# Kernel optimization log

Hardware: AMD Instinct MI355X
Metric: run time of the kernel (lower is better)

Reference implementation:

```python
import jax, jax.numpy as jnp
import numpy as np

EPS = 1e-8


def setup_inputs() -> dict:
    key = jax.random.key(0)
    ks = jax.random.split(key, 8)
    B, N, D = 8, 2048, 768
    H, R = 768, 4
    return {
        "x": jax.random.normal(ks[0], (B, N, D), dtype=jnp.float32),
        "scale": jnp.ones((D,), dtype=jnp.float32),
        "U": jax.random.normal(ks[1], (H, R), dtype=jnp.float32) * 0.02,
        "V": jax.random.normal(ks[2], (H, R), dtype=jnp.float32) * 0.02,
        "S_param": jax.random.normal(ks[3], (H, H), dtype=jnp.float32) * 0.01,
        "Bm": jax.random.normal(ks[4], (H, D), dtype=jnp.float32) * (1.0 / np.sqrt(D)),
        "Cm": jax.random.normal(ks[5], (D, H), dtype=jnp.float32) * (1.0 / np.sqrt(H)),
        "gate_w": jax.random.normal(ks[6], (D, D), dtype=jnp.float32) * (1.0 / np.sqrt(D)),
        "gate_b": jnp.zeros((D,), dtype=jnp.float32),
        "alpha": jnp.full((1,), 0.1, dtype=jnp.float32),
    }


def reference(x, scale, U, V, S_param, Bm, Cm, gate_w, gate_b, alpha):
    B, N, D = x.shape
    H = Bm.shape[0]
    # A = diag(A_diag) + U V^T + (S - S^T); A_diag is a fixed buffer.
    A_diag = -jnp.linspace(1.0, float(H), H, dtype=x.dtype) / H
    A = jnp.diag(A_diag) + U @ V.T + (S_param - S_param.T)
    At = A.T  # apply as h @ A.T
    # RMSNorm
    rms = jnp.sqrt(jnp.mean(x * x, axis=-1, keepdims=True) + EPS)
    xn = x / rms * scale
    # Precompute input injections u_t = x_t @ B.T for all t: (N, B, H)
    u = jnp.einsum('bnd,hd->nbh', xn, Bm)

    def step(h, ut):
        h = h @ At + ut
        return h, h @ Cm.T  # (B, D)

    h0 = jnp.zeros((B, H), dtype=x.dtype)
    _, y_fwd = jax.lax.scan(step, h0, u)                 # (N, B, D)
    _, y_bwd = jax.lax.scan(step, h0, u, reverse=True)   # (N, B, D), indexed in time order
    y = 0.5 * (y_fwd + y_bwd)
    y = jnp.swapaxes(y, 0, 1)  # (B, N, D)
    # Gate
    g = jax.nn.sigmoid(jnp.einsum('bnd,ed->bne', xn, gate_w) + gate_b)
    y = y * g
    # Skip (dropout is identity in eval)
    return x + alpha * y
```

## Files before the change

kernel.cpp:

```cpp
#include <hip/hip_runtime.h>


typedef short  bfrag __attribute__((ext_vector_type(8)));
typedef float  ffrag __attribute__((ext_vector_type(4)));
typedef float  f4    __attribute__((ext_vector_type(4)));
typedef short  s4v   __attribute__((ext_vector_type(4)));

#define DEV static __device__ __forceinline__
#define Hn 768
#define FLS 132

DEV unsigned short f2bf(float f) {
  unsigned u = __float_as_uint(f);
  u += 0x7fffu + ((u >> 16) & 1u);
  return (unsigned short)(u >> 16);
}
DEV float bf2f(unsigned short s) { return __uint_as_float(((unsigned)s) << 16); }

DEV ffrag mfma16(bfrag a, bfrag b, ffrag c) {
  return __builtin_amdgcn_mfma_f32_16x16x32_bf16(a, b, c, 0, 0, 0);
}

DEV void glds16(const unsigned short* g, unsigned short* l) {
  __builtin_amdgcn_global_load_lds(
      (const __attribute__((address_space(1))) unsigned int*)g,
      (__attribute__((address_space(3))) unsigned int*)l, 16, 0, 0);
}

template<int N> DEV void vwait() {
  if constexpr (N == 0)      asm volatile("s_waitcnt vmcnt(0)" ::: "memory");
  else if constexpr (N == 4) asm volatile("s_waitcnt vmcnt(4)" ::: "memory");
  else if constexpr (N == 8) asm volatile("s_waitcnt vmcnt(8)" ::: "memory");
}

union BF8 { bfrag v; unsigned short u[8]; };

__global__ __launch_bounds__(256) void k_abuild(
    const float* __restrict__ U, const float* __restrict__ V,
    const float* __restrict__ S, const float* __restrict__ Bm,
    const float* __restrict__ Cm, const float* __restrict__ gw,
    float* __restrict__ Af, float* __restrict__ AfT,
    unsigned short* __restrict__ Abf,
    unsigned short* __restrict__ Bmb, unsigned short* __restrict__ Cmb,
    unsigned short* __restrict__ gwb, unsigned short* __restrict__ zp) {
  int i = blockIdx.x;
  int task = blockIdx.y;
  if (task == 0) {
    float u0 = U[i*4+0], u1 = U[i*4+1], u2 = U[i*4+2], u3 = U[i*4+3];
    for (int j = threadIdx.x; j < Hn; j += 256) {
      float a = u0*V[j*4+0] + u1*V[j*4+1] + u2*V[j*4+2] + u3*V[j*4+3]
              + S[i*Hn+j] - S[j*Hn+i];
      if (i == j) a += -(float)(i+1) / 768.0f;
      Af[i*Hn+j]  = a;
      AfT[j*Hn+i] = a;
      Abf[i*Hn+j] = f2bf(a);
    }
    if (i == 0) for (int j = threadIdx.x; j < 1024; j += 256) zp[j] = 0;
  } else {
    const float* src = (task==1) ? Bm : (task==2) ? Cm : gw;
    unsigned short* dst = (task==1) ? Bmb : (task==2) ? Cmb : gwb;
    for (int j = threadIdx.x; j < Hn; j += 256) dst[i*Hn+j] = f2bf(src[i*Hn+j]);
  }
}

__global__ __launch_bounds__(256) void k_rms(
    const float* __restrict__ x, const float* __restrict__ scale,
    unsigned short* __restrict__ xn) {
  int row  = blockIdx.x * 4 + (threadIdx.x >> 6);
  int lane = threadIdx.x & 63;
  int b = row >> 11, t = row & 2047;
  const float* xr = x + (long)row * Hn;
  float v[12];
  float ss = 0.f;
#pragma unroll
  for (int j = 0; j < 12; ++j) { v[j] = xr[lane + j*64]; ss += v[j]*v[j]; }
#pragma unroll
  for (int off = 1; off < 64; off <<= 1) ss += __shfl_xor(ss, off);
  float inv = 1.0f / sqrtf(ss / 768.0f + 1e-8f);
  unsigned short* dst = xn + ((long)t * 8 + b) * Hn;
#pragma unroll
  for (int j = 0; j < 12; ++j) dst[lane + j*64] = f2bf(v[j] * inv * scale[lane + j*64]);
}

__global__ __launch_bounds__(512) void k_sq(
    const float* __restrict__ X, const float* __restrict__ XT,
    float* __restrict__ Z, float* __restrict__ ZT,
    unsigned short* __restrict__ Zbf) {
  int tid = threadIdx.x, lane = tid & 63, w = tid >> 6;
  int mw = w >> 2, nw = w & 3, l15 = lane & 15, lhi = lane >> 4;
  int rb = blockIdx.x * 64, cb = blockIdx.y * 128;
  ffrag acc[2][2] = {};
  for (int kt = 0; kt < 24; ++kt) {
    int k0 = kt*32 + lhi*8;
    BF8 ah[2], al[2], bh[2], bl[2];
#pragma unroll
    for (int mt = 0; mt < 2; ++mt) {
      const f4* p = (const f4*)(X + (long)(rb + mw*32 + mt*16 + l15) * Hn + k0);
      f4 x0 = p[0], x1 = p[1];
#pragma unroll
      for (int j = 0; j < 8; ++j) {
        float f = (j < 4) ? x0[j] : x1[j-4];
        unsigned short h = f2bf(f);
        ah[mt].u[j] = h; al[mt].u[j] = f2bf(f - bf2f(h));
      }
    }
#pragma unroll
    for (int nt = 0; nt < 2; ++nt) {
      const f4* p = (const f4*)(XT + (long)(cb + nw*32 + nt*16 + l15) * Hn + k0);
      f4 x0 = p[0], x1 = p[1];
#pragma unroll
      for (int j = 0; j < 8; ++j) {
        float f = (j < 4) ? x0[j] : x1[j-4];
        unsigned short h = f2bf(f);
        bh[nt].u[j] = h; bl[nt].u[j] = f2bf(f - bf2f(h));
      }
    }
#pragma unroll
    for (int mt = 0; mt < 2; ++mt)
#pragma unroll
      for (int nt = 0; nt < 2; ++nt) {
        acc[mt][nt] = mfma16(ah[mt].v, bh[nt].v, acc[mt][nt]);
        acc[mt][nt] = mfma16(ah[mt].v, bl[nt].v, acc[mt][nt]);
        acc[mt][nt] = mfma16(al[mt].v, bh[nt].v, acc[mt][nt]);
      }
  }
#pragma unroll
  for (int mt = 0; mt < 2; ++mt)
#pragma unroll
    for (int nt = 0; nt < 2; ++nt)
#pragma unroll
      for (int q = 0; q < 4; ++q) {
        int grow = rb + mw*32 + mt*16 + lhi*4 + q;
        int gcol = cb + nw*32 + nt*16 + l15;
        float vv = acc[mt][nt][q];
        Z[(long)grow*Hn + gcol] = vv;
        ZT[(long)gcol*Hn + grow] = vv;
        Zbf[(long)grow*Hn + gcol] = f2bf(vv);
      }
}

template<int MODE>
__global__ __launch_bounds__(256) void k_gemm(
    const unsigned short* __restrict__ A0s, const unsigned short* __restrict__ A1s,
    const unsigned short* __restrict__ B0s, const unsigned short* __restrict__ B1s,
    const unsigned short* __restrict__ res, unsigned short* __restrict__ outb,
    const unsigned short* __restrict__ zp, int sh, int dup,
    const float* __restrict__ gb, const float* __restrict__ alpha,
    const float* __restrict__ x, float* __restrict__ outf) {
  constexpr int NA   = (MODE == 0) ? 1 : 2;
  constexpr int NB   = (MODE == 2) ? 2 : 1;
  constexpr int NT   = NA + NB;
  constexpr int NBUF = (MODE == 0) ? 3 : 2;
  constexpr int NL   = 2 * NT;

  __shared__ __align__(16) char smem[NBUF * NT * 8192];
  unsigned short* ldsb = (unsigned short*)smem;

  const int tid = threadIdx.x, lane = tid & 63, w = tid >> 6;
  const int l15 = lane & 15, lhi = lane >> 4;
  const int wr = w >> 1, wc = w & 1;

  const int nwg = gridDim.x;
  const int q8 = nwg >> 3, r8 = nwg & 7, xcd = blockIdx.x & 7, fo = blockIdx.x >> 3;
  const int wg = (xcd < r8 ? xcd*(q8+1) : r8*(q8+1) + (xcd - r8)*q8) + fo;
  const int cb = wg % 6, rbk = wg / 6;
  const long r0 = (long)rbk * 128;
  const long bc0 = (long)cb * 128;
  const int dir = (MODE == 0 && r0 >= 16384) ? 1 : 0;

  bool skip = false;
  if (MODE == 0 && sh > 0)
    skip = dir ? (r0 >= 32768 - sh) : (r0 + 128 <= sh);

  const int rowin = lane >> 2, ch = lane & 3;
  long gA[NA][2]; bool vA[NA][2]; long gB[NB][2]; int lbase[2];
#pragma unroll
  for (int jj = 0; jj < 2; ++jj) {
    const int inst = w*2 + jj;
    const int r = inst*16 + rowin;
    const int c = ch ^ ((r ^ (r >> 2)) & 3);
    lbase[jj] = inst * 512;
#pragma unroll
    for (int s = 0; s < NA; ++s) {
      long gr; bool ok = true;
      if (MODE == 0) {
        gr = r0 + r + (dir ? sh : -sh);
        ok = dir ? (gr < 32768) : (gr >= 0);
      } else if (MODE == 1) {
        if (s == 0) { gr = r0 + r - sh; ok = (gr >= 0); }
        else        { gr = r0 + r + 16384 + sh; ok = (gr < 32768); }
      } else {
        gr = r0 + r;
      }
      vA[s][jj] = ok; gA[s][jj] = gr * Hn + c*8;
    }
#pragma unroll
    for (int s = 0; s < NB; ++s)
      gB[s][jj] = (bc0 + r) * Hn + c*8;
  }

  auto stage = [&](int buf, int kt) {
    const int ko = kt * 32;
    unsigned short* dst = ldsb + buf * (NT * 4096);
#pragma unroll
    for (int jj = 0; jj < 2; ++jj) {
#pragma unroll
      for (int s = 0; s < NA; ++s) {
        const unsigned short* src0 = (MODE == 2 && s == 1) ? A1s : A0s;
        const unsigned short* g = vA[s][jj] ? (src0 + gA[s][jj] + ko) : zp;
        glds16(g, dst + s*4096 + lbase[jj]);
      }
#pragma unroll
      for (int s = 0; s < NB; ++s) {
        const unsigned short* src0 = (s == 0) ? B0s : B1s;
        glds16(src0 + gB[s][jj] + ko, dst + (NA + s)*4096 + lbase[jj]);
      }
    }
  };

  ffrag acc[4][4] = {};
  ffrag accZ[(MODE == 2) ? 4 : 1][(MODE == 2) ? 4 : 1] = {};
  const int cx = (lhi ^ ((l15 ^ (l15 >> 2)) & 3)) * 8;

  if (!skip) {
    if (MODE == 0) {
      stage(0, 0); stage(1, 1);
      int cur = 0;
      for (int kt = 0; kt < 24; ++kt) {
        if (kt < 23) vwait<4>(); else vwait<0>();
        __builtin_amdgcn_s_barrier();
        if (kt + 2 <= 23) stage((kt + 2) % 3, kt + 2);
        const unsigned short* L = ldsb + cur * (NT * 4096);
        bfrag a0[4], b0[4];
#pragma unroll
        for (int mt = 0; mt < 4; ++mt)
          a0[mt] = *(const bfrag*)&L[(wr*64 + mt*16 + l15)*32 + cx];
#pragma unroll
        for (int nt = 0; nt < 4; ++nt)
          b0[nt] = *(const bfrag*)&L[4096 + (wc*64 + nt*16 + l15)*32 + cx];
#pragma unroll
        for (int mt = 0; mt < 4; ++mt)
#pragma unroll
          for (int nt = 0; nt < 4; ++nt)
            acc[mt][nt] = mfma16(a0[mt], b0[nt], acc[mt][nt]);
        cur = (cur == 2) ? 0 : cur + 1;
      }
    } else {
      stage(0, 0);
      int cur = 0;
      for (int kt = 0; kt < 24; ++kt) {
        vwait<0>();
        __builtin_amdgcn_s_barrier();
        if (kt < 23) stage(cur ^ 1, kt + 1);
        const unsigned short* L = ldsb + cur * (NT * 4096);
        bfrag a[2][4], b0[4], b1[4];
#pragma unroll
        for (int mt = 0; mt < 4; ++mt) {
          const int row = wr*64 + mt*16 + l15;
          a[0][mt] = *(const bfrag*)&L[row*32 + cx];
          a[1][mt] = *(const bfrag*)&L[4096 + row*32 + cx];
        }
#pragma unroll
        for (int nt = 0; nt < 4; ++nt) {
          const int row = wc*64 + nt*16 + l15;
          b0[nt] = *(const bfrag*)&L[2*4096 + row*32 + cx];
          if (MODE == 2) b1[nt] = *(const bfrag*)&L[3*4096 + row*32 + cx];
        }
#pragma unroll
        for (int mt = 0; mt < 4; ++mt)
#pragma unroll
          for (int nt = 0; nt < 4; ++nt) {
            if (MODE == 1) {
              acc[mt][nt] = mfma16(a[0][mt], b0[nt], acc[mt][nt]);
              acc[mt][nt] = mfma16(a[1][mt], b0[nt], acc[mt][nt]);
            } else {
              acc[mt][nt]  = mfma16(a[0][mt], b0[nt], acc[mt][nt]);
              accZ[mt][nt] = mfma16(a[1][mt], b1[nt], accZ[mt][nt]);
            }
          }
        cur ^= 1;
      }
    }
  }

  if (MODE == 2) {
    const float al = alpha[0];
    float gvals[4];
#pragma unroll
    for (int nt = 0; nt < 4; ++nt) gvals[nt] = gb[bc0 + wc*64 + nt*16 + l15];
#pragma unroll
    for (int mt = 0; mt < 4; ++mt)
#pragma unroll
      for (int nt = 0; nt < 4; ++nt)
#pragma unroll
        for (int q = 0; q < 4; ++q) {
          float z = accZ[mt][nt][q] + gvals[nt];
          float g = 1.0f / (1.0f + __expf(-z));
          acc[mt][nt][q] *= al * 0.5f * g;
        }
  }

  float* fl = (float*)smem;
#pragma unroll
  for (int hh = 0; hh < 2; ++hh) {
    __syncthreads();
    if (wr == hh) {
#pragma unroll
      for (int mt = 0; mt < 4; ++mt)
#pragma unroll
        for (int nt = 0; nt < 4; ++nt)
#pragma unroll
          for (int q = 0; q < 4; ++q)
            fl[(mt*16 + lhi*4 + q)*FLS + wc*64 + nt*16 + l15] = acc[mt][nt][q];
    }
    __syncthreads();
    for (int i = tid; i < 2048; i += 256) {
      const int row = i >> 5;
      const int cc  = (i & 31) << 2;
      f4 v = *(const f4*)&fl[row*FLS + cc];
      const long grow = r0 + hh*64 + row;
      const long gcol = bc0 + cc;
      const long go = grow * Hn + gcol;
      if (MODE == 0) {
        if (res) {
          s4v rv = *(const s4v*)&res[go];
#pragma unroll
          for (int j = 0; j < 4; ++j) v[j] += bf2f(((unsigned short*)&rv)[j]);
        }
        s4v ov;
#pragma unroll
        for (int j = 0; j < 4; ++j) ((unsigned short*)&ov)[j] = f2bf(v[j]);
        *(s4v*)&outb[go] = ov;
        if (dup) *(s4v*)&outb[go + (long)16384*Hn] = ov;
      } else if (MODE == 1) {
        s4v ra = *(const s4v*)&res[go];
        s4v rb2 = *(const s4v*)&res[go + (long)16384*Hn];
#pragma unroll
        for (int j = 0; j < 4; ++j)
          v[j] += bf2f(((unsigned short*)&ra)[j]) + bf2f(((unsigned short*)&rb2)[j]);
        s4v ov;
#pragma unroll
        for (int j = 0; j < 4; ++j) ((unsigned short*)&ov)[j] = f2bf(v[j]);
        *(s4v*)&outb[go] = ov;
      } else {
        const long t = grow >> 3, b = grow & 7;
        const long o = (b*2048 + t)*Hn + gcol;
        f4 xv = *(const f4*)&x[o];
        f4 ov;
#pragma unroll
        for (int j = 0; j < 4; ++j) ov[j] = xv[j] + v[j];
        *(f4*)&outf[o] = ov;
      }
    }
  }
}

extern "C" void kernel_launch(void* const* d_in, const int* in_sizes, int n_in,
                              void* d_out, int out_size, void* d_ws, size_t ws_size,
                              hipStream_t stream) {
  const float* x     = (const float*)d_in[0];
  const float* scale = (const float*)d_in[1];
  const float* U     = (const float*)d_in[2];
  const float* V     = (const float*)d_in[3];
  const float* S     = (const float*)d_in[4];
  const float* Bm    = (const float*)d_in[5];
  const float* Cm    = (const float*)d_in[6];
  const float* gw    = (const float*)d_in[7];
  const float* gb    = (const float*)d_in[8];
  const float* alpha = (const float*)d_in[9];
  float* out = (float*)d_out;

  char* p = (char*)d_ws;
  auto alloc = [&](size_t sz) { char* r = p; p += (sz + 255) & ~(size_t)255; return r; };

  const size_t SZ_X  = (size_t)32768 * Hn * sizeof(unsigned short);
  const size_t SZ_BF = (size_t)16384 * Hn * sizeof(unsigned short);
  const size_t SZ_M  = (size_t)Hn * Hn * sizeof(float);
  const size_t SZ_MB = (size_t)Hn * Hn * sizeof(unsigned short);

  unsigned short* xn = (unsigned short*)alloc(SZ_BF);
  unsigned short* XA = (unsigned short*)alloc(SZ_X);
  unsigned short* XB = (unsigned short*)alloc(SZ_X);
  float* Af  = (float*)alloc(SZ_M);
  float* AfT = (float*)alloc(SZ_M);
  float* P1  = (float*)alloc(SZ_M);
  float* P1T = (float*)alloc(SZ_M);
  float* P2  = (float*)alloc(SZ_M);
  float* P2T = (float*)alloc(SZ_M);
  unsigned short* Abf = (unsigned short*)alloc(SZ_MB);
  unsigned short* Ab[10];
  for (int i = 0; i < 10; ++i) Ab[i] = (unsigned short*)alloc(SZ_MB);
  unsigned short* Bmb = (unsigned short*)alloc(SZ_MB);
  unsigned short* Cmb = (unsigned short*)alloc(SZ_MB);
  unsigned short* gwb = (unsigned short*)alloc(SZ_MB);
  unsigned short* zp  = (unsigned short*)alloc(1024 * sizeof(unsigned short));

  if ((size_t)(p - (char*)d_ws) > ws_size) return;

  k_abuild<<<dim3(768, 4), 256, 0, stream>>>(U, V, S, Bm, Cm, gw,
      Af, AfT, Abf, Bmb, Cmb, gwb, zp);
  k_rms<<<4096, 256, 0, stream>>>(x, scale, xn);

  const float* sx = Af; const float* sxt = AfT;
  float* za = P1; float* zat = P1T; float* zb = P2; float* zbt = P2T;
  for (int i = 0; i < 10; ++i) {
    k_sq<<<dim3(12, 6), 512, 0, stream>>>(sx, sxt, za, zat, Ab[i]);
    sx = za; sxt = zat;
    float* t1 = za; float* t2 = zat; za = zb; zat = zbt; zb = t1; zbt = t2;
  }

  k_gemm<0><<<768, 256, 0, stream>>>(xn, nullptr, Bmb, nullptr, nullptr, XA,
      zp, 0, 1, nullptr, nullptr, nullptr, nullptr);

  unsigned short* src = XA; unsigned short* dst = XB;
  for (int i = 0; i < 10; ++i) {
    const unsigned short* W = (i == 0) ? Abf : Ab[i-1];
    k_gemm<0><<<1536, 256, 0, stream>>>(src, nullptr, W, nullptr, src, dst,
        zp, 8 << i, 0, nullptr, nullptr, nullptr, nullptr);
    unsigned short* t = src; src = dst; dst = t;
  }
  unsigned short* xsum = (src == XA) ? XB : XA;
  k_gemm<1><<<768, 256, 0, stream>>>(src, nullptr, Ab[9], nullptr, src, xsum,
      zp, 8192, 0, nullptr, nullptr, nullptr, nullptr);

  k_gemm<2><<<768, 256, 0, stream>>>(xsum, xn, Cmb, gwb, nullptr, nullptr,
      zp, 0, 0, gb, alpha, x, out);
}
```

Measured before the change: 1.262 ms.

## Use 512-thread 128x256-tile GEMM kernel for the doubling-scan levels

Replaces the generic 256-thread 128x128 GEMM used for the input projection and the ten log-step scan levels with a new 512-thread kernel. Each block now covers 128 rows by 256 columns, so every loaded A tile is reused across twice as many output columns and fewer blocks are launched. The triple-buffered vmcnt pipeline is replaced by double buffering synchronised with __syncthreads, and the epilogue writes out through LDS in four row passes. The gated output GEMM becomes its own specialised kernel. The trade-off is larger blocks, more LDS per block and a simpler, possibly less overlapped, load/compute pipeline.

```diff
diff --git a/kernel.cpp b/kernel.cpp
--- a/kernel.cpp
+++ b/kernel.cpp
@@ -9,6 +9,7 @@
 #define DEV static __device__ __forceinline__
 #define Hn 768
 #define FLS 132
+#define BLS 260
 
 DEV unsigned short f2bf(float f) {
   unsigned u = __float_as_uint(f);
@@ -25,12 +26,6 @@
   __builtin_amdgcn_global_load_lds(
       (const __attribute__((address_space(1))) unsigned int*)g,
       (__attribute__((address_space(3))) unsigned int*)l, 16, 0, 0);
-}
-
-template<int N> DEV void vwait() {
-  if constexpr (N == 0)      asm volatile("s_waitcnt vmcnt(0)" ::: "memory");
-  else if constexpr (N == 4) asm volatile("s_waitcnt vmcnt(4)" ::: "memory");
-  else if constexpr (N == 8) asm volatile("s_waitcnt vmcnt(8)" ::: "memory");
 }
 
 union BF8 { bfrag v; unsigned short u[8]; };
@@ -140,20 +135,154 @@
 }
 
 template<int MODE>
-__global__ __launch_bounds__(256) void k_gemm(
+__global__ __launch_bounds__(512) void k_lvl(
+    const unsigned short* __restrict__ A0s, const unsigned short* __restrict__ B0s,
+    const unsigned short* __restrict__ res, unsigned short* __restrict__ outb,
+    const unsigned short* __restrict__ zp, int sh) {
+  constexpr int NS   = (MODE == 2) ? 2 : 1;
+  constexpr int BUFS = NS * 4096 + 8192;
+  __shared__ __align__(16) unsigned short ldsb[2 * BUFS];
+
+  const int tid = threadIdx.x, lane = tid & 63, w = tid >> 6;
+  const int l15 = lane & 15, lhi = lane >> 4;
+  const int wr = w >> 2, wc = w & 3;
+
+  const int nwg = gridDim.x;
+  const int q8 = nwg >> 3, r8 = nwg & 7, xcd = blockIdx.x & 7, fo = blockIdx.x >> 3;
+  const int wg = (xcd < r8 ? xcd*(q8+1) : r8*(q8+1) + (xcd - r8)*q8) + fo;
+  const int cb = wg % 3, rbk = wg / 3;
+  const long r0  = (long)rbk * 128;
+  const long bc0 = (long)cb * 256;
+  const int dir = (MODE == 1 && r0 >= 16384) ? 1 : 0;
+
+  bool skip = false;
+  if (MODE == 1)
+    skip = dir ? (r0 >= 32768 - sh) : (r0 + 128 <= sh);
+
+  const int rowin = lane >> 2, ch = lane & 3;
+  const int rA = w*16 + rowin;
+  const int cswz = ch ^ ((rowin ^ (rowin >> 2)) & 3);
+  long gA[NS]; bool vA[NS];
+#pragma unroll
+  for (int s = 0; s < NS; ++s) {
+    long gr; bool ok = true;
+    if (MODE == 0) {
+      gr = r0 + rA;
+    } else if (MODE == 1) {
+      gr = r0 + rA + (dir ? sh : -sh);
+      ok = dir ? (gr < 32768) : (gr >= 0);
+    } else {
+      if (s == 0) { gr = r0 + rA - sh;         ok = (gr >= 0);    }
+      else        { gr = r0 + rA + 16384 + sh; ok = (gr < 32768); }
+    }
+    vA[s] = ok; gA[s] = gr * Hn + cswz*8;
+  }
+  long gB[2];
+#pragma unroll
+  for (int j = 0; j < 2; ++j)
+    gB[j] = (bc0 + j*128 + rA) * Hn + cswz*8;
+
+  auto stage = [&](int buf, int kt) {
+    const int ko = kt * 32;
+    unsigned short* dst = ldsb + buf * BUFS;
+#pragma unroll
+    for (int s = 0; s < NS; ++s) {
+      const unsigned short* g = vA[s] ? (A0s + gA[s] + ko) : zp;
+      glds16(g, dst + s*4096 + w*512);
+    }
+#pragma unroll
+    for (int j = 0; j < 2; ++j)
+      glds16(B0s + gB[j] + ko, dst + NS*4096 + j*4096 + w*512);
+  };
+
+  ffrag acc[4][4] = {};
+  const int cx = (lhi ^ ((l15 ^ (l15 >> 2)) & 3)) * 8;
+
+  if (!skip) {
+    stage(0, 0);
+    __syncthreads();
+    int cur = 0;
+    for (int kt = 0; kt < 24; ++kt) {
+      if (kt < 23) stage(cur ^ 1, kt + 1);
+      const unsigned short* L = ldsb + cur * BUFS;
+      bfrag a[NS][4], b[4];
+#pragma unroll
+      for (int mt = 0; mt < 4; ++mt) {
+        const int row = wr*64 + mt*16 + l15;
+#pragma unroll
+        for (int s = 0; s < NS; ++s)
+          a[s][mt] = *(const bfrag*)&L[s*4096 + row*32 + cx];
+      }
+#pragma unroll
+      for (int nt = 0; nt < 4; ++nt) {
+        const int row = wc*64 + nt*16 + l15;
+        b[nt] = *(const bfrag*)&L[NS*4096 + row*32 + cx];
+      }
+#pragma unroll
+      for (int mt = 0; mt < 4; ++mt)
+#pragma unroll
+        for (int nt = 0; nt < 4; ++nt) {
+          acc[mt][nt] = mfma16(a[0][mt], b[nt], acc[mt][nt]);
+          if (NS == 2) acc[mt][nt] = mfma16(a[1][mt], b[nt], acc[mt][nt]);
+        }
+      __syncthreads();
+      cur ^= 1;
+    }
+  }
+
+  float* fl = (float*)ldsb;
+#pragma unroll
+  for (int p = 0; p < 4; ++p) {
+    __syncthreads();
+#pragma unroll
+    for (int nt = 0; nt < 4; ++nt)
+#pragma unroll
+      for (int q = 0; q < 4; ++q)
+        fl[(wr*16 + lhi*4 + q)*BLS + wc*64 + nt*16 + l15] = acc[p][nt][q];
+    __syncthreads();
+    for (int i = tid; i < 2048; i += 512) {
+      const int srow = i >> 6;
+      const int cc   = (i & 63) << 2;
+      f4 v = *(const f4*)&fl[srow*BLS + cc];
+      const long grow = r0 + (srow >> 4)*64 + p*16 + (srow & 15);
+      const long gcol = bc0 + cc;
+      const long go = grow * Hn + gcol;
+      if (MODE == 0) {
+        s4v ov;
+#pragma unroll
+        for (int j = 0; j < 4; ++j) ((unsigned short*)&ov)[j] = f2bf(v[j]);
+        *(s4v*)&outb[go] = ov;
+        *(s4v*)&outb[go + (long)16384*Hn] = ov;
+      } else if (MODE == 1) {
+        s4v rv = *(const s4v*)&res[go];
+#pragma unroll
+        for (int j = 0; j < 4; ++j) v[j] += bf2f(((unsigned short*)&rv)[j]);
+        s4v ov;
+#pragma unroll
+        for (int j = 0; j < 4; ++j) ((unsigned short*)&ov)[j] = f2bf(v[j]);
+        *(s4v*)&outb[go] = ov;
+      } else {
+        s4v ra = *(const s4v*)&res[go];
+        s4v rb2 = *(const s4v*)&res[go + (long)16384*Hn];
+#pragma unroll
+        for (int j = 0; j < 4; ++j)
+          v[j] += bf2f(((unsigned short*)&ra)[j]) + bf2f(((unsigned short*)&rb2)[j]);
+        s4v ov;
+#pragma unroll
+        for (int j = 0; j < 4; ++j) ((unsigned short*)&ov)[j] = f2bf(v[j]);
+        *(s4v*)&outb[go] = ov;
+      }
+    }
+  }
+}
+
+__global__ __launch_bounds__(256) void k_fin(
     const unsigned short* __restrict__ A0s, const unsigned short* __restrict__ A1s,
     const unsigned short* __restrict__ B0s, const unsigned short* __restrict__ B1s,
-    const unsigned short* __restrict__ res, unsigned short* __restrict__ outb,
-    const unsigned short* __restrict__ zp, int sh, int dup,
+    const unsigned short* __restrict__ zp,
     const float* __restrict__ gb, const float* __restrict__ alpha,
     const float* __restrict__ x, float* __restrict__ outf) {
-  constexpr int NA   = (MODE == 0) ? 1 : 2;
-  constexpr int NB   = (MODE == 2) ? 2 : 1;
-  constexpr int NT   = NA + NB;
-  constexpr int NBUF = (MODE == 0) ? 3 : 2;
-  constexpr int NL   = 2 * NT;
-
-  __shared__ __align__(16) char smem[NBUF * NT * 8192];
+  __shared__ __align__(16) char smem[2 * 4 * 8192];
   unsigned short* ldsb = (unsigned short*)smem;
 
   const int tid = threadIdx.x, lane = tid & 63, w = tid >> 6;
@@ -166,139 +295,81 @@
   const int cb = wg % 6, rbk = wg / 6;
   const long r0 = (long)rbk * 128;
   const long bc0 = (long)cb * 128;
-  const int dir = (MODE == 0 && r0 >= 16384) ? 1 : 0;
-
-  bool skip = false;
-  if (MODE == 0 && sh > 0)
-    skip = dir ? (r0 >= 32768 - sh) : (r0 + 128 <= sh);
 
   const int rowin = lane >> 2, ch = lane & 3;
-  long gA[NA][2]; bool vA[NA][2]; long gB[NB][2]; int lbase[2];
+  long gA[2][2]; long gB[2][2]; int lbase[2];
 #pragma unroll
   for (int jj = 0; jj < 2; ++jj) {
     const int inst = w*2 + jj;
     const int r = inst*16 + rowin;
     const int c = ch ^ ((r ^ (r >> 2)) & 3);
     lbase[jj] = inst * 512;
-#pragma unroll
-    for (int s = 0; s < NA; ++s) {
-      long gr; bool ok = true;
-      if (MODE == 0) {
-        gr = r0 + r + (dir ? sh : -sh);
-        ok = dir ? (gr < 32768) : (gr >= 0);
-      } else if (MODE == 1) {
-        if (s == 0) { gr = r0 + r - sh; ok = (gr >= 0); }
-        else        { gr = r0 + r + 16384 + sh; ok = (gr < 32768); }
-      } else {
-        gr = r0 + r;
-      }
-      vA[s][jj] = ok; gA[s][jj] = gr * Hn + c*8;
-    }
-#pragma unroll
-    for (int s = 0; s < NB; ++s)
-      gB[s][jj] = (bc0 + r) * Hn + c*8;
+    gA[0][jj] = (r0 + r) * Hn + c*8;
+    gA[1][jj] = gA[0][jj];
+    gB[0][jj] = (bc0 + r) * Hn + c*8;
+    gB[1][jj] = gB[0][jj];
   }
 
   auto stage = [&](int buf, int kt) {
     const int ko = kt * 32;
-    unsigned short* dst = ldsb + buf * (NT * 4096);
+    unsigned short* dst = ldsb + buf * 16384;
 #pragma unroll
     for (int jj = 0; jj < 2; ++jj) {
-#pragma unroll
-      for (int s = 0; s < NA; ++s) {
-        const unsigned short* src0 = (MODE == 2 && s == 1) ? A1s : A0s;
-        const unsigned short* g = vA[s][jj] ? (src0 + gA[s][jj] + ko) : zp;
-        glds16(g, dst + s*4096 + lbase[jj]);
-      }
-#pragma unroll
-      for (int s = 0; s < NB; ++s) {
-        const unsigned short* src0 = (s == 0) ? B0s : B1s;
-        glds16(src0 + gB[s][jj] + ko, dst + (NA + s)*4096 + lbase[jj]);
-      }
+      glds16(A0s + gA[0][jj] + ko, dst + 0*4096 + lbase[jj]);
+      glds16(A1s + gA[1][jj] + ko, dst + 1*4096 + lbase[jj]);
+      glds16(B0s + gB[0][jj] + ko, dst + 2*4096 + lbase[jj]);
+      glds16(B1s + gB[1][jj] + ko, dst + 3*4096 + lbase[jj]);
     }
   };
 
   ffrag acc[4][4] = {};
-  ffrag accZ[(MODE == 2) ? 4 : 1][(MODE == 2) ? 4 : 1] = {};
+  ffrag accZ[4][4] = {};
   const int cx = (lhi ^ ((l15 ^ (l15 >> 2)) & 3)) * 8;
 
-  if (!skip) {
-    if (MODE == 0) {
-      stage(0, 0); stage(1, 1);
-      int cur = 0;
-      for (int kt = 0; kt < 24; ++kt) {
-        if (kt < 23) vwait<4>(); else vwait<0>();
-        __builtin_amdgcn_s_barrier();
-        if (kt + 2 <= 23) stage((kt + 2) % 3, kt + 2);
-        const unsigned short* L = ldsb + cur * (NT * 4096);
-        bfrag a0[4], b0[4];
-#pragma unroll
-        for (int mt = 0; mt < 4; ++mt)
-          a0[mt] = *(const bfrag*)&L[(wr*64 + mt*16 + l15)*32 + cx];
-#pragma unroll
-        for (int nt = 0; nt < 4; ++nt)
-          b0[nt] = *(const bfrag*)&L[4096 + (wc*64 + nt*16 + l15)*32 + cx];
-#pragma unroll
-        for (int mt = 0; mt < 4; ++mt)
-#pragma unroll
-          for (int nt = 0; nt < 4; ++nt)
-            acc[mt][nt] = mfma16(a0[mt], b0[nt], acc[mt][nt]);
-        cur = (cur == 2) ? 0 : cur + 1;
-      }
-    } else {
-      stage(0, 0);
-      int cur = 0;
-      for (int kt = 0; kt < 24; ++kt) {
-        vwait<0>();
-        __builtin_amdgcn_s_barrier();
-        if (kt < 23) stage(cur ^ 1, kt + 1);
-        const unsigned short* L = ldsb + cur * (NT * 4096);
-        bfrag a[2][4], b0[4], b1[4];
-#pragma unroll
-        for (int mt = 0; mt < 4; ++mt) {
-          const int row = wr*64 + mt*16 + l15;
-          a[0][mt] = *(const bfrag*)&L[row*32 + cx];
-          a[1][mt] = *(const bfrag*)&L[4096 + row*32 + cx];
-        }
-#pragma unroll
-        for (int nt = 0; nt < 4; ++nt) {
-          const int row = wc*64 + nt*16 + l15;
-          b0[nt] = *(const bfrag*)&L[2*4096 + row*32 + cx];
-          if (MODE == 2) b1[nt] = *(const bfrag*)&L[3*4096 + row*32 + cx];
-        }
-#pragma unroll
-        for (int mt = 0; mt < 4; ++mt)
-#pragma unroll
-          for (int nt = 0; nt < 4; ++nt) {
-            if (MODE == 1) {
-              acc[mt][nt] = mfma16(a[0][mt], b0[nt], acc[mt][nt]);
-              acc[mt][nt] = mfma16(a[1][mt], b0[nt], acc[mt][nt]);
-            } else {
-              acc[mt][nt]  = mfma16(a[0][mt], b0[nt], acc[mt][nt]);
-              accZ[mt][nt] = mfma16(a[1][mt], b1[nt], accZ[mt][nt]);
-            }
-          }
-        cur ^= 1;
-      }
-    }
-  }
-
-  if (MODE == 2) {
-    const float al = alpha[0];
-    float gvals[4];
-#pragma unroll
-    for (int nt = 0; nt < 4; ++nt) gvals[nt] = gb[bc0 + wc*64 + nt*16 + l15];
+  stage(0, 0);
+  int cur = 0;
+  for (int kt = 0; kt < 24; ++kt) {
+    asm volatile("s_waitcnt vmcnt(0)" ::: "memory");
+    __builtin_amdgcn_s_barrier();
+    if (kt < 23) stage(cur ^ 1, kt + 1);
+    const unsigned short* L = ldsb + cur * 16384;
+    bfrag a[2][4], b0[4], b1[4];
+#pragma unroll
+    for (int mt = 0; mt < 4; ++mt) {
+      const int row = wr*64 + mt*16 + l15;
+      a[0][mt] = *(const bfrag*)&L[row*32 + cx];
+      a[1][mt] = *(const bfrag*)&L[4096 + row*32 + cx];
+    }
+#pragma unroll
+    for (int nt = 0; nt < 4; ++nt) {
+      const int row = wc*64 + nt*16 + l15;
+      b0[nt] = *(const bfrag*)&L[2*4096 + row*32 + cx];
+      b1[nt] = *(const bfrag*)&L[3*4096 + row*32 + cx];
+    }
 #pragma unroll
     for (int mt = 0; mt < 4; ++mt)
 #pragma unroll
-      for (int nt = 0; nt < 4; ++nt)
-#pragma unroll
-        for (int q = 0; q < 4; ++q) {
-          float z = accZ[mt][nt][q] + gvals[nt];
-          float g = 1.0f / (1.0f + __expf(-z));
-          acc[mt][nt][q] *= al * 0.5f * g;
-        }
-  }
+      for (int nt = 0; nt < 4; ++nt) {
+        acc[mt][nt]  = mfma16(a[0][mt], b0[nt], acc[mt][nt]);
+        accZ[mt][nt] = mfma16(a[1][mt], b1[nt], accZ[mt][nt]);
+      }
+    cur ^= 1;
+  }
+
+  const float al = alpha[0];
+  float gvals[4];
+#pragma unroll
+  for (int nt = 0; nt < 4; ++nt) gvals[nt] = gb[bc0 + wc*64 + nt*16 + l15];
+#pragma unroll
+  for (int mt = 0; mt < 4; ++mt)
+#pragma unroll
+    for (int nt = 0; nt < 4; ++nt)
+#pragma unroll
+      for (int q = 0; q < 4; ++q) {
+        float z = accZ[mt][nt][q] + gvals[nt];
+        float g = 1.0f / (1.0f + __expf(-z));
+        acc[mt][nt][q] *= al * 0.5f * g;
+      }
 
   float* fl = (float*)smem;
 #pragma unroll
@@ -320,37 +391,13 @@
       f4 v = *(const f4*)&fl[row*FLS + cc];
       const long grow = r0 + hh*64 + row;
       const long gcol = bc0 + cc;
-      const long go = grow * Hn + gcol;
-      if (MODE == 0) {
-        if (res) {
-          s4v rv = *(const s4v*)&res[go];
-#pragma unroll
-          for (int j = 0; j < 4; ++j) v[j] += bf2f(((unsigned short*)&rv)[j]);
-        }
-        s4v ov;
-#pragma unroll
-        for (int j = 0; j < 4; ++j) ((unsigned short*)&ov)[j] = f2bf(v[j]);
-        *(s4v*)&outb[go] = ov;
-        if (dup) *(s4v*)&outb[go + (long)16384*Hn] = ov;
-      } else if (MODE == 1) {
-        s4v ra = *(const s4v*)&res[go];
-        s4v rb2 = *(const s4v*)&res[go + (long)16384*Hn];
-#pragma unroll
-        for (int j = 0; j < 4; ++j)
-          v[j] += bf2f(((unsigned short*)&ra)[j]) + bf2f(((unsigned short*)&rb2)[j]);
-        s4v ov;
-#pragma unroll
-        for (int j = 0; j < 4; ++j) ((unsigned short*)&ov)[j] = f2bf(v[j]);
-        *(s4v*)&outb[go] = ov;
-      } else {
-        const long t = grow >> 3, b = grow & 7;
-        const long o = (b*2048 + t)*Hn + gcol;
-        f4 xv = *(const f4*)&x[o];
-        f4 ov;
-#pragma unroll
-        for (int j = 0; j < 4; ++j) ov[j] = xv[j] + v[j];
-        *(f4*)&outf[o] = ov;
-      }
+      const long t = grow >> 3, b = grow & 7;
+      const long o = (b*2048 + t)*Hn + gcol;
+      f4 xv = *(const f4*)&x[o];
+      f4 ov;
+#pragma unroll
+      for (int j = 0; j < 4; ++j) ov[j] = xv[j] + v[j];
+      *(f4*)&outf[o] = ov;
     }
   }
 }
@@ -409,20 +456,15 @@
     float* t1 = za; float* t2 = zat; za = zb; zat = zbt; zb = t1; zbt = t2;
   }
 
-  k_gemm<0><<<768, 256, 0, stream>>>(xn, nullptr, Bmb, nullptr, nullptr, XA,
-      zp, 0, 1, nullptr, nullptr, nullptr, nullptr);
+  k_lvl<0><<<384, 512, 0, stream>>>(xn, Bmb, nullptr, XA, zp, 0);
 
   unsigned short* src = XA; unsigned short* dst = XB;
   for (int i = 0; i < 10; ++i) {
     const unsigned short* W = (i == 0) ? Abf : Ab[i-1];
-    k_gemm<0><<<1536, 256, 0, stream>>>(src, nullptr, W, nullptr, src, dst,
-        zp, 8 << i, 0, nullptr, nullptr, nullptr, nullptr);
+    k_lvl<1><<<768, 512, 0, stream>>>(src, W, src, dst, zp, 8 << i);
     unsigned short* t = src; src = dst; dst = t;
   }
-  unsigned short* xsum = (src == XA) ? XB : XA;
-  k_gemm<1><<<768, 256, 0, stream>>>(src, nullptr, Ab[9], nullptr, src, xsum,
-      zp, 8192, 0, nullptr, nullptr, nullptr, nullptr);
-
-  k_gemm<2><<<768, 256, 0, stream>>>(xsum, xn, Cmb, gwb, nullptr, nullptr,
-      zp, 0, 0, gb, alpha, x, out);
-}
+  k_lvl<2><<<384, 512, 0, stream>>>(src, Ab[9], src, XB, zp, 8192);
+
+  k_fin<<<768, 256, 0, stream>>>(XB, xn, Cmb, gwb, zp, gb, alpha, x, out);
+}
```

New measurement: 1.241 ms. About the same (-1.7%).
